# Kernel tuning notes

Hardware: AMD Instinct MI355X
Metric: run time of the kernel (lower is better)

Reference implementation:

```python
import jax, jax.numpy as jnp
import numpy as np

B, V, E = 64, 16384, 524288          # batch cells, genes (graph nodes), edges
CL1_F, CL1_K = 32, 6                  # cheby conv out-features, polynomial order
POOL = 8
FC1Fin = CL1_F * (V // POOL)          # 65536
FC1_F, FC2_F = 512, 512
NN_FC1, NN_FC2 = 1024, 512
OUT = 10


def _linear_params(k, fout, fin):
    k1, k2 = jax.random.split(k)
    s = 1.0 / np.sqrt(fin)
    w = jax.random.uniform(k1, (fout, fin), minval=-s, maxval=s, dtype=jnp.float32)
    b = jax.random.uniform(k2, (fout,), minval=-s, maxval=s, dtype=jnp.float32)
    return w, b


def setup_inputs() -> dict:
    key = jax.random.key(0)
    ks = jax.random.split(key, 12)
    cl1_w, cl1_b = _linear_params(ks[0], CL1_F, CL1_K)
    fc1_w, fc1_b = _linear_params(ks[1], FC1_F, FC1Fin)
    fc2_w, fc2_b = _linear_params(ks[2], FC2_F, FC1_F)
    fc3_w, fc3_b = _linear_params(ks[3], V, FC2_F)
    nn1_w, nn1_b = _linear_params(ks[4], NN_FC1, V)
    nn2_w, nn2_b = _linear_params(ks[5], NN_FC2, NN_FC1)
    sum2_w, sum2_b = _linear_params(ks[6], OUT, FC1_F + NN_FC2)
    x_in = jax.random.normal(ks[7], (B, V), dtype=jnp.float32)
    L_rows = jax.random.randint(ks[8], (E,), 0, V, dtype=jnp.int32)
    L_cols = jax.random.randint(ks[9], (E,), 0, V, dtype=jnp.int32)
    # values of the rescaled Laplacian 2L/lmax - I (preprocessing done on host)
    L_vals = jax.random.normal(ks[10], (E,), dtype=jnp.float32) * 0.01
    return dict(x_in=x_in, L_vals=L_vals,
                cl1_w=cl1_w, cl1_b=cl1_b, fc1_w=fc1_w, fc1_b=fc1_b,
                fc2_w=fc2_w, fc2_b=fc2_b, fc3_w=fc3_w, fc3_b=fc3_b,
                nn1_w=nn1_w, nn1_b=nn1_b, nn2_w=nn2_w, nn2_b=nn2_b,
                sum2_w=sum2_w, sum2_b=sum2_b,
                L_rows=L_rows, L_cols=L_cols)


def _spmm(vals, rows, cols, x):
    # sparse [V,V] @ dense [V,B] via gather + segment_sum
    return jax.ops.segment_sum(vals[:, None] * x[cols], rows, num_segments=V)


def reference(x_in, L_vals, cl1_w, cl1_b, fc1_w, fc1_b, fc2_w, fc2_b,
              fc3_w, fc3_b, nn1_w, nn1_b, nn2_w, nn2_b, sum2_w, sum2_b,
              L_rows, L_cols):
    # --- graph_conv_cheby (Fin = 1) ---
    x0 = x_in.T                      # [V, B]  (== view of [V, Fin*B])
    xs = [x0]
    x1 = _spmm(L_vals, L_rows, L_cols, x0)
    xs.append(x1)
    for _ in range(2, CL1_K):
        x2 = 2.0 * _spmm(L_vals, L_rows, L_cols, x1) - x0
        xs.append(x2)
        x0, x1 = x1, x2
    xc = jnp.stack(xs, 0)            # [K, V, B]
    xc = xc.transpose(2, 1, 0)       # [B, V, K]
    x = xc @ cl1_w.T + cl1_b         # [B, V, CL1_F]
    x = jax.nn.relu(x)
    # --- graph_max_pool(p=8) over node dim ---
    x = x.reshape(B, V // POOL, POOL, CL1_F).max(axis=2)   # [B, V/8, CL1_F]
    x = x.reshape(B, FC1Fin)
    # --- GAE hidden + decode branch ---
    x_hidden = jax.nn.relu(x @ fc1_w.T + fc1_b)            # [B, FC1_F]
    xd = jax.nn.relu(x_hidden @ fc2_w.T + fc2_b)           # FC2_F != 0 path
    # Dropout(d) with d=0 -> identity (deterministic reference)
    x_decode = xd @ fc3_w.T + fc3_b                        # [B, V]
    # --- plain NN branch on raw input ---
    xn = jax.nn.relu(x_in @ nn1_w.T + nn1_b)
    xn = jax.nn.relu(xn @ nn2_w.T + nn2_b)                 # [B, NN_FC2]
    # --- fuse + classify ---
    xcat = jnp.concatenate([x_hidden, xn], axis=1)
    logp = jax.nn.log_softmax(xcat @ sum2_w.T + sum2_b, axis=1)  # [B, OUT]
    return x_decode, x_hidden, logp
```

## Files before the change

kernel.cpp:

```cpp
#include <hip/hip_runtime.h>

#define B_    64
#define V_    16384
#define E_    524288
#define KCH   6
#define FCH   32
#define FIN1  65536
#define FC1F  512
#define FC2F  512
#define NN1F  1024
#define NN2F  512
#define OUTC  10
#define KT2   64

#define OFF_XS      0u
#define OFF_SCOL    12582912u
#define OFF_SVAL    13631488u
#define OFF_RSTART  14680064u
#define OFF_CNT     14746112u
#define OFF_CF      14811648u
#define OFF_SLICE   15073792u
#define OFF_XD      15073792u
#define OFF_XN1     15204864u
#define OFF_XN2     15467008u

typedef __attribute__((ext_vector_type(4))) float v4f;
typedef __attribute__((ext_vector_type(2))) float v2f;
typedef __attribute__((ext_vector_type(4))) unsigned short u16x4;

__device__ __forceinline__ float b2f(unsigned short h) {
    union { unsigned int u; float f; } v; v.u = ((unsigned int)h) << 16; return v.f;
}
__device__ __forceinline__ unsigned short f2b(float f) {
    union { float f; unsigned int u; } v; v.f = f;
    unsigned int u = v.u;
    u += 0x7fffu + ((u >> 16) & 1u);
    return (unsigned short)(u >> 16);
}

__global__ void prep_k(const float* __restrict__ xin, unsigned short* __restrict__ x0) {
    __shared__ unsigned short tl[64][65];
    int t = threadIdx.x;
    int v0 = blockIdx.x * 64;
    #pragma unroll
    for (int i = 0; i < 16; i++) {
        int idx = t + i * 256;
        int b = idx >> 6, v = idx & 63;
        tl[v][b] = f2b(xin[(size_t)b * V_ + v0 + v]);
    }
    __syncthreads();
    #pragma unroll
    for (int i = 0; i < 16; i++) {
        int idx = t + i * 256;
        int v = idx >> 6, b = idx & 63;
        x0[(size_t)(v0 + v) * B_ + b] = tl[v][b];
    }
}

__global__ void count_k(const int* __restrict__ rows, int* __restrict__ cnt) {
    int e = blockIdx.x * 256 + threadIdx.x;
    if (e < E_) atomicAdd(&cnt[rows[e] & (V_ - 1)], 1);
}

__global__ void scan_k(int* __restrict__ cnt_cursor, int* __restrict__ row_start) {
    __shared__ int sums[256];
    int t = threadIdx.x;
    int loc[64];
    int s = 0;
    #pragma unroll
    for (int i = 0; i < 64; i++) { loc[i] = cnt_cursor[t * 64 + i]; s += loc[i]; }
    sums[t] = s;
    __syncthreads();
    for (int off = 1; off < 256; off <<= 1) {
        int v = (t >= off) ? sums[t - off] : 0;
        __syncthreads();
        sums[t] += v;
        __syncthreads();
    }
    int base = (t == 0) ? 0 : sums[t - 1];
    #pragma unroll
    for (int i = 0; i < 64; i++) {
        row_start[t * 64 + i] = base;
        cnt_cursor[t * 64 + i] = base;
        base += loc[i];
    }
    if (t == 255) row_start[V_] = base;
}

__global__ void scatter_k(const int* __restrict__ rows, const int* __restrict__ cols,
                          const float* __restrict__ vals,
                          int* __restrict__ cursor, unsigned short* __restrict__ scol,
                          unsigned short* __restrict__ sval) {
    int e = blockIdx.x * 256 + threadIdx.x;
    if (e < E_) {
        int r = rows[e] & (V_ - 1);
        int p = atomicAdd(&cursor[r], 1);
        scol[p] = (unsigned short)(cols[e] & (V_ - 1));
        sval[p] = f2b(vals[e]);
    }
}

__global__ void spmm_k(const int* __restrict__ row_start, const unsigned short* __restrict__ scol,
                       const unsigned short* __restrict__ sval,
                       const unsigned short* __restrict__ x,
                       const unsigned short* __restrict__ xprev, unsigned short* __restrict__ y,
                       int mode) {
    int row  = blockIdx.x * 4 + (threadIdx.x >> 6);
    int lane = threadIdx.x & 63;
    int s = row_start[row], e = row_start[row + 1];
    float a0 = 0.f, a1 = 0.f, a2 = 0.f, a3 = 0.f;
    int i = s;
    for (; i + 4 <= e; i += 4) {
        int c0 = scol[i], c1 = scol[i + 1], c2 = scol[i + 2], c3 = scol[i + 3];
        float v0 = b2f(sval[i]), v1 = b2f(sval[i + 1]);
        float v2 = b2f(sval[i + 2]), v3 = b2f(sval[i + 3]);
        a0 += v0 * b2f(x[(size_t)c0 * B_ + lane]);
        a1 += v1 * b2f(x[(size_t)c1 * B_ + lane]);
        a2 += v2 * b2f(x[(size_t)c2 * B_ + lane]);
        a3 += v3 * b2f(x[(size_t)c3 * B_ + lane]);
    }
    for (; i < e; i++)
        a0 += b2f(sval[i]) * b2f(x[(size_t)scol[i] * B_ + lane]);
    float acc = (a0 + a1) + (a2 + a3);
    size_t o = (size_t)row * B_ + lane;
    float r = mode ? (2.f * acc - b2f(xprev[o])) : acc;
    y[o] = f2b(r);
}

__global__ void cheby_slice_k(const unsigned short* __restrict__ xs, const float* __restrict__ w,
                              const float* __restrict__ bias, unsigned short* __restrict__ slice,
                              int g) {
    __shared__ float tile[KCH * 512];
    __shared__ float wf[FCH * KCH];
    __shared__ float bf[FCH];
    int t = threadIdx.x;
    int vpl = blockIdx.x;
    int vp = g * 256 + vpl;
    for (int i = t; i < KCH * 512; i += 256) {
        int k = i >> 9, rem = i & 511;
        tile[i] = b2f(xs[(size_t)k * V_ * B_ + (size_t)vp * 512 + rem]);
    }
    if (t < FCH * KCH) wf[t] = w[t];
    if (t < FCH) bf[t] = bias[t];
    __syncthreads();
    int f = t & 31, b0 = t >> 5;
    float wr[KCH];
    #pragma unroll
    for (int k = 0; k < KCH; k++) wr[k] = wf[f * KCH + k];
    float bb = bf[f];
    #pragma unroll
    for (int bi = 0; bi < 8; bi++) {
        int b = b0 * 8 + bi;
        float m = -1e30f;
        #pragma unroll
        for (int j = 0; j < 8; j++) {
            float s = bb;
            #pragma unroll
            for (int k = 0; k < KCH; k++) s += tile[k * 512 + j * 64 + b] * wr[k];
            m = fmaxf(m, s);
        }
        slice[(size_t)b * 8192 + vpl * FCH + f] = f2b(fmaxf(m, 0.f));
    }
}

__global__ void gemm3_k(const void* __restrict__ Av, int a32, int lda, int ka0,
                        const float* __restrict__ W, int ldw, int kw0,
                        int klen, int N, const float* __restrict__ bias,
                        int relu, int direct, int accum,
                        float* __restrict__ Cp, float* __restrict__ Co) {
    __shared__ float As[KT2][68];
    __shared__ float Ws[KT2][36];
    const unsigned short* Au = (const unsigned short*)Av;
    const float* Af = (const float*)Av;
    int t = threadIdx.x;
    int nb = blockIdx.x * 32;
    int ka = ka0 + blockIdx.y * klen;
    int kw = kw0 + blockIdx.y * klen;
    int kq = t & 15;
    int r0 = t >> 4;
    int tm = (t & 31) << 1;
    int tn = (t >> 5) << 2;
    float acc[2][4] = {{0.f, 0.f, 0.f, 0.f}, {0.f, 0.f, 0.f, 0.f}};
    for (int kt = 0; kt < klen; kt += KT2) {
        __syncthreads();
        int kk = kq << 2;
        #pragma unroll
        for (int p = 0; p < 4; p++) {
            int row = r0 + p * 16;
            float a0, a1, a2, a3;
            if (a32) {
                v4f v = *(const v4f*)(Af + (size_t)row * lda + ka + kt + kk);
                a0 = v[0]; a1 = v[1]; a2 = v[2]; a3 = v[3];
            } else {
                u16x4 h = *(const u16x4*)(Au + (size_t)row * lda + ka + kt + kk);
                a0 = b2f(h[0]); a1 = b2f(h[1]); a2 = b2f(h[2]); a3 = b2f(h[3]);
            }
            As[kk + 0][row] = a0; As[kk + 1][row] = a1;
            As[kk + 2][row] = a2; As[kk + 3][row] = a3;
        }
        #pragma unroll
        for (int p = 0; p < 2; p++) {
            int row = r0 + p * 16;
            v4f w = *(const v4f*)(W + (size_t)(nb + row) * ldw + kw + kt + kk);
            Ws[kk + 0][row] = w[0]; Ws[kk + 1][row] = w[1];
            Ws[kk + 2][row] = w[2]; Ws[kk + 3][row] = w[3];
        }
        __syncthreads();
        #pragma unroll 8
        for (int k = 0; k < KT2; k++) {
            v2f a = *(const v2f*)&As[k][tm];
            v4f w = *(const v4f*)&Ws[k][tn];
            #pragma unroll
            for (int i = 0; i < 2; i++)
                #pragma unroll
                for (int j = 0; j < 4; j++)
                    acc[i][j] += a[i] * w[j];
        }
    }
    if (direct) {
        #pragma unroll
        for (int i = 0; i < 2; i++) {
            int m = tm + i;
            v4f v;
            #pragma unroll
            for (int j = 0; j < 4; j++) {
                float x = acc[i][j] + bias[nb + tn + j];
                v[j] = relu ? fmaxf(x, 0.f) : x;
            }
            *(v4f*)(Co + (size_t)m * N + nb + tn) = v;
        }
    } else {
        float* base = Cp + (size_t)blockIdx.y * 64 * N;
        #pragma unroll
        for (int i = 0; i < 2; i++) {
            int m = tm + i;
            float* p = base + (size_t)m * N + nb + tn;
            v4f v;
            if (accum) {
                v4f old = *(const v4f*)p;
                #pragma unroll
                for (int j = 0; j < 4; j++) v[j] = old[j] + acc[i][j];
            } else {
                #pragma unroll
                for (int j = 0; j < 4; j++) v[j] = acc[i][j];
            }
            *(v4f*)p = v;
        }
    }
}

__global__ void finish2_k(const float* __restrict__ Cp, int Y, int len,
                          const float* __restrict__ bias, int nmask, int relu,
                          float* __restrict__ o) {
    int i = blockIdx.x * 256 + threadIdx.x;
    float s = bias[i & nmask];
    for (int y = 0; y < Y; y++) s += Cp[(size_t)y * len + i];
    if (relu) s = fmaxf(s, 0.f);
    o[i] = s;
}

__global__ void sum2_k(const float* __restrict__ xh, const float* __restrict__ xn,
                       const float* __restrict__ w, const float* __restrict__ bias,
                       float* __restrict__ out) {
    int b = blockIdx.x;
    int lane = threadIdx.x;
    float xc[16];
    #pragma unroll
    for (int j = 0; j < 8; j++) xc[j] = xh[b * FC1F + j * 64 + lane];
    #pragma unroll
    for (int j = 0; j < 8; j++) xc[8 + j] = xn[b * NN2F + j * 64 + lane];
    float logits[OUTC];
    #pragma unroll
    for (int o = 0; o < OUTC; o++) {
        float s = 0.f;
        #pragma unroll
        for (int j = 0; j < 16; j++) s += xc[j] * w[o * 1024 + j * 64 + lane];
        #pragma unroll
        for (int off = 32; off; off >>= 1) s += __shfl_xor(s, off);
        logits[o] = s + bias[o];
    }
    float mx = logits[0];
    #pragma unroll
    for (int o = 1; o < OUTC; o++) mx = fmaxf(mx, logits[o]);
    float lse = 0.f;
    #pragma unroll
    for (int o = 0; o < OUTC; o++) lse += expf(logits[o] - mx);
    float lg = logf(lse) + mx;
    if (lane < OUTC) out[b * OUTC + lane] = logits[lane] - lg;
}

extern "C" void kernel_launch(void* const* d_in, const int* in_sizes, int n_in,
                              void* d_out, int out_size, void* d_ws, size_t ws_size,
                              hipStream_t stream) {
    const float* x_in   = (const float*)d_in[0];
    const float* L_vals = (const float*)d_in[1];
    const float* cl1_w  = (const float*)d_in[2];
    const float* cl1_b  = (const float*)d_in[3];
    const float* fc1_w  = (const float*)d_in[4];
    const float* fc1_b  = (const float*)d_in[5];
    const float* fc2_w  = (const float*)d_in[6];
    const float* fc2_b  = (const float*)d_in[7];
    const float* fc3_w  = (const float*)d_in[8];
    const float* fc3_b  = (const float*)d_in[9];
    const float* nn1_w  = (const float*)d_in[10];
    const float* nn1_b  = (const float*)d_in[11];
    const float* nn2_w  = (const float*)d_in[12];
    const float* nn2_b  = (const float*)d_in[13];
    const float* sum2_w = (const float*)d_in[14];
    const float* sum2_b = (const float*)d_in[15];
    const int* L_rows = (const int*)d_in[16];
    const int* L_cols = (const int*)d_in[17];
    float* out = (float*)d_out;
    char* ws = (char*)d_ws;

    unsigned short* xs     = (unsigned short*)(ws + OFF_XS);
    unsigned short* scol   = (unsigned short*)(ws + OFF_SCOL);
    unsigned short* sval   = (unsigned short*)(ws + OFF_SVAL);
    int*            rstart = (int*)(ws + OFF_RSTART);
    int*            cnt    = (int*)(ws + OFF_CNT);
    unsigned short* slice  = (unsigned short*)(ws + OFF_SLICE);
    float*          xd     = (float*)(ws + OFF_XD);
    float*          xn1    = (float*)(ws + OFF_XN1);
    float*          xn2    = (float*)(ws + OFF_XN2);
    float*          cp_a   = (float*)(ws + OFF_SCOL);
    float*          cp_b   = (float*)(ws + OFF_XS);

    float* out_decode = out;
    float* out_hidden = out + (size_t)B_ * V_;
    float* out_logp   = out_hidden + B_ * FC1F;

    prep_k<<<V_ / 64, 256, 0, stream>>>(x_in, xs);

    hipMemsetAsync(cnt, 0, V_ * sizeof(int), stream);
    count_k<<<E_ / 256, 256, 0, stream>>>(L_rows, cnt);
    scan_k<<<1, 256, 0, stream>>>(cnt, rstart);
    scatter_k<<<E_ / 256, 256, 0, stream>>>(L_rows, L_cols, L_vals, cnt, scol, sval);

    size_t VB = (size_t)V_ * B_;
    spmm_k<<<V_ / 4, 256, 0, stream>>>(rstart, scol, sval, xs, nullptr, xs + VB, 0);
    for (int k = 2; k < KCH; k++)
        spmm_k<<<V_ / 4, 256, 0, stream>>>(rstart, scol, sval,
                                           xs + (k - 1) * VB, xs + (k - 2) * VB, xs + k * VB, 1);

    for (int g = 0; g < 8; g++) {
        cheby_slice_k<<<256, 256, 0, stream>>>(xs, cl1_w, cl1_b, slice, g);
        gemm3_k<<<dim3(FC1F / 32, 16), 256, 0, stream>>>(slice, 0, 8192, 0,
                                                         fc1_w, FIN1, g * 8192,
                                                         512, FC1F, nullptr, 0, 0, g ? 1 : 0,
                                                         cp_a, nullptr);
    }
    finish2_k<<<B_ * FC1F / 256, 256, 0, stream>>>(cp_a, 16, B_ * FC1F, fc1_b, FC1F - 1, 1, out_hidden);

    gemm3_k<<<dim3(FC2F / 32, 8), 256, 0, stream>>>(out_hidden, 1, FC1F, 0,
                                                    fc2_w, FC1F, 0,
                                                    64, FC2F, nullptr, 0, 0, 0, cp_a, nullptr);
    finish2_k<<<B_ * FC2F / 256, 256, 0, stream>>>(cp_a, 8, B_ * FC2F, fc2_b, FC2F - 1, 1, xd);

    gemm3_k<<<dim3(V_ / 32, 1), 256, 0, stream>>>(xd, 1, FC2F, 0,
                                                  fc3_w, FC2F, 0,
                                                  FC2F, V_, fc3_b, 0, 1, 0, nullptr, out_decode);

    gemm3_k<<<dim3(NN1F / 32, 32), 256, 0, stream>>>(x_in, 1, V_, 0,
                                                     nn1_w, V_, 0,
                                                     512, NN1F, nullptr, 0, 0, 0, cp_b, nullptr);
    finish2_k<<<B_ * NN1F / 256, 256, 0, stream>>>(cp_b, 32, B_ * NN1F, nn1_b, NN1F - 1, 1, xn1);

    gemm3_k<<<dim3(NN2F / 32, 16), 256, 0, stream>>>(xn1, 1, NN1F, 0,
                                                     nn2_w, NN1F, 0,
                                                     64, NN2F, nullptr, 0, 0, 0, cp_b, nullptr);
    finish2_k<<<B_ * NN2F / 256, 256, 0, stream>>>(cp_b, 16, B_ * NN2F, nn2_b, NN2F - 1, 1, xn2);

    sum2_k<<<B_, 64, 0, stream>>>(out_hidden, xn2, sum2_w, sum2_b, out_logp);
}
```

Baseline: 870.6 us.

## Merge pipeline into three cooperative persistent kernels synchronized with grid barriers

Replaces about thirty separate launches (prep, CSR build, five SpMM steps, the eight cheby/fc1 rounds, the back-end GEMMs and reductions) with three cooperative kernels of 512 blocks that move between stages through grid.sync. The split-K for fc1 is re-partitioned so each block keeps its accumulator in registers across all eight slices and writes its partials only once, with the reduction fused in. The aim is to remove launch gaps and per-round partial-sum traffic. In exchange, the SpMM and GEMM stages are limited to 512 resident blocks and pay for many grid barriers. The old launch sequence is kept as a fallback if a cooperative launch fails.

```diff
diff --git a/kernel.cpp b/kernel.cpp
--- a/kernel.cpp
+++ b/kernel.cpp
@@ -1,4 +1,7 @@
 #include <hip/hip_runtime.h>
+#include <hip/hip_cooperative_groups.h>
+
+namespace cg = cooperative_groups;
 
 #define B_    64
 #define V_    16384
@@ -18,7 +21,6 @@
 #define OFF_SVAL    13631488u
 #define OFF_RSTART  14680064u
 #define OFF_CNT     14746112u
-#define OFF_CF      14811648u
 #define OFF_SLICE   15073792u
 #define OFF_XD      15073792u
 #define OFF_XN1     15204864u
@@ -38,6 +40,367 @@
     return (unsigned short)(u >> 16);
 }
 
+template <int A32>
+__device__ __forceinline__ void gemm_block(const void* __restrict__ Av, int lda, int ka,
+                                           const float* __restrict__ W, int ldw, int kw,
+                                           int klen, int nb, char* smem,
+                                           float acc[2][4], int t) {
+    float* As = (float*)smem;
+    float* Ws = (float*)(smem + KT2 * 68 * 4);
+    const unsigned short* Au = (const unsigned short*)Av;
+    const float* Af = (const float*)Av;
+    int kq = t & 15, r0 = t >> 4;
+    int tm = (t & 31) << 1, tn = (t >> 5) << 2;
+    for (int kt = 0; kt < klen; kt += KT2) {
+        __syncthreads();
+        int kk = kq << 2;
+        #pragma unroll
+        for (int p = 0; p < 4; p++) {
+            int row = r0 + p * 16;
+            float a0, a1, a2, a3;
+            if (A32) {
+                v4f v = *(const v4f*)(Af + (size_t)row * lda + ka + kt + kk);
+                a0 = v[0]; a1 = v[1]; a2 = v[2]; a3 = v[3];
+            } else {
+                u16x4 h = *(const u16x4*)(Au + (size_t)row * lda + ka + kt + kk);
+                a0 = b2f(h[0]); a1 = b2f(h[1]); a2 = b2f(h[2]); a3 = b2f(h[3]);
+            }
+            As[(kk + 0) * 68 + row] = a0; As[(kk + 1) * 68 + row] = a1;
+            As[(kk + 2) * 68 + row] = a2; As[(kk + 3) * 68 + row] = a3;
+        }
+        #pragma unroll
+        for (int p = 0; p < 2; p++) {
+            int row = r0 + p * 16;
+            v4f w = *(const v4f*)(W + (size_t)(nb + row) * ldw + kw + kt + kk);
+            Ws[(kk + 0) * 36 + row] = w[0]; Ws[(kk + 1) * 36 + row] = w[1];
+            Ws[(kk + 2) * 36 + row] = w[2]; Ws[(kk + 3) * 36 + row] = w[3];
+        }
+        __syncthreads();
+        #pragma unroll 8
+        for (int k = 0; k < KT2; k++) {
+            v2f a = *(const v2f*)&As[k * 68 + tm];
+            v4f w = *(const v4f*)&Ws[k * 36 + tn];
+            #pragma unroll
+            for (int i = 0; i < 2; i++)
+                #pragma unroll
+                for (int j = 0; j < 4; j++)
+                    acc[i][j] += a[i] * w[j];
+        }
+    }
+}
+
+
+__global__ void __launch_bounds__(256, 2) front_coop_k(
+        const float* __restrict__ xin, const int* __restrict__ rows,
+        const int* __restrict__ cols, const float* __restrict__ vals,
+        unsigned short* __restrict__ xs, unsigned short* __restrict__ scol,
+        unsigned short* __restrict__ sval, int* __restrict__ rstart,
+        int* __restrict__ cnt) {
+    cg::grid_group grid = cg::this_grid();
+    int t = threadIdx.x;
+    int bx = blockIdx.x;
+    __shared__ __align__(16) unsigned short tl[64][66];
+    __shared__ int sums[256];
+
+    if (bx < 256) {
+        int v0 = bx * 64;
+        #pragma unroll
+        for (int i = 0; i < 16; i++) {
+            int idx = t + i * 256;
+            int b = idx >> 6, v = idx & 63;
+            tl[v][b] = f2b(xin[(size_t)b * V_ + v0 + v]);
+        }
+        __syncthreads();
+        #pragma unroll
+        for (int i = 0; i < 16; i++) {
+            int idx = t + i * 256;
+            int v = idx >> 6, b = idx & 63;
+            xs[(size_t)(v0 + v) * B_ + b] = tl[v][b];
+        }
+    } else if (bx < 320) {
+        cnt[(bx - 256) * 256 + t] = 0;
+    }
+    grid.sync();
+
+    {
+        int idx = bx * 256 + t;
+        #pragma unroll
+        for (int h = 0; h < 4; h++)
+            atomicAdd(&cnt[rows[idx + h * 131072] & (V_ - 1)], 1);
+    }
+    grid.sync();
+
+    if (bx == 0) {
+        int s = 0;
+        for (int i = 0; i < 64; i++) s += cnt[t * 64 + i];
+        sums[t] = s;
+        __syncthreads();
+        for (int off = 1; off < 256; off <<= 1) {
+            int v = (t >= off) ? sums[t - off] : 0;
+            __syncthreads();
+            sums[t] += v;
+            __syncthreads();
+        }
+        int base = (t == 0) ? 0 : sums[t - 1];
+        for (int i = 0; i < 64; i++) {
+            int idx = t * 64 + i;
+            int c = cnt[idx];
+            rstart[idx] = base;
+            cnt[idx] = base;
+            base += c;
+        }
+        if (t == 255) rstart[V_] = base;
+    }
+    grid.sync();
+
+    {
+        int idx = bx * 256 + t;
+        #pragma unroll
+        for (int h = 0; h < 4; h++) {
+            int e = idx + h * 131072;
+            int r = rows[e] & (V_ - 1);
+            int p = atomicAdd(&cnt[r], 1);
+            scol[p] = (unsigned short)(cols[e] & (V_ - 1));
+            sval[p] = f2b(vals[e]);
+        }
+    }
+    grid.sync();
+
+    size_t VB = (size_t)V_ * B_;
+    int lane = t & 63;
+    int w = t >> 6;
+    for (int k = 1; k < KCH; k++) {
+        const unsigned short* x = xs + (size_t)(k - 1) * VB;
+        const unsigned short* xprev = xs + (size_t)(k >= 2 ? k - 2 : 0) * VB;
+        unsigned short* y = xs + (size_t)k * VB;
+        for (int rr = 0; rr < 8; rr++) {
+            int row = bx * 32 + w * 8 + rr;
+            int s = rstart[row], e = rstart[row + 1];
+            float a0 = 0.f, a1 = 0.f, a2 = 0.f, a3 = 0.f;
+            int i = s;
+            for (; i + 4 <= e; i += 4) {
+                int c0 = scol[i], c1 = scol[i + 1], c2 = scol[i + 2], c3 = scol[i + 3];
+                float v0 = b2f(sval[i]), v1 = b2f(sval[i + 1]);
+                float v2 = b2f(sval[i + 2]), v3 = b2f(sval[i + 3]);
+                a0 += v0 * b2f(x[(size_t)c0 * B_ + lane]);
+                a1 += v1 * b2f(x[(size_t)c1 * B_ + lane]);
+                a2 += v2 * b2f(x[(size_t)c2 * B_ + lane]);
+                a3 += v3 * b2f(x[(size_t)c3 * B_ + lane]);
+            }
+            for (; i < e; i++)
+                a0 += b2f(sval[i]) * b2f(x[(size_t)scol[i] * B_ + lane]);
+            float acc = (a0 + a1) + (a2 + a3);
+            size_t o = (size_t)row * B_ + lane;
+            float r = (k >= 2) ? (2.f * acc - b2f(xprev[o])) : acc;
+            y[o] = f2b(r);
+        }
+        if (k < KCH - 1) grid.sync();
+    }
+}
+
+__global__ void __launch_bounds__(256, 2) fc1_coop_k(
+        const unsigned short* __restrict__ xs, const float* __restrict__ cw,
+        const float* __restrict__ cb, const float* __restrict__ fw,
+        const float* __restrict__ fb, unsigned short* __restrict__ slice,
+        float* __restrict__ cp, float* __restrict__ outh) {
+    cg::grid_group grid = cg::this_grid();
+    int t = threadIdx.x;
+    int bx = blockIdx.x;
+    __shared__ __align__(16) char smem[26624];
+    size_t VB = (size_t)V_ * B_;
+
+    float acc[2][4] = {{0.f, 0.f, 0.f, 0.f}, {0.f, 0.f, 0.f, 0.f}};
+    int nb = (bx & 15) * 32;
+    int y  = bx >> 4;
+
+    for (int g = 0; g < 8; g++) {
+        {
+            float* tile = (float*)smem;
+            float* wf   = tile + KCH * 512;
+            float* bf   = wf + FCH * KCH;
+            int vpl = bx >> 1;
+            int bhalf = bx & 1;
+            int vp = g * 256 + vpl;
+            for (int i = t; i < KCH * 512; i += 256) {
+                int k = i >> 9, rem = i & 511;
+                tile[i] = b2f(xs[(size_t)k * VB + (size_t)vp * 512 + rem]);
+            }
+            if (t < FCH * KCH) wf[t] = cw[t];
+            if (t < FCH) bf[t] = cb[t];
+            __syncthreads();
+            int f = t & 31, b0 = t >> 5;
+            float wr[KCH];
+            #pragma unroll
+            for (int k = 0; k < KCH; k++) wr[k] = wf[f * KCH + k];
+            float bb = bf[f];
+            #pragma unroll
+            for (int bi2 = 0; bi2 < 4; bi2++) {
+                int bi = bhalf * 4 + bi2;
+                int b = b0 * 8 + bi;
+                float m = -1e30f;
+                #pragma unroll
+                for (int j = 0; j < 8; j++) {
+                    float s = bb;
+                    #pragma unroll
+                    for (int k = 0; k < KCH; k++) s += tile[k * 512 + j * 64 + b] * wr[k];
+                    m = fmaxf(m, s);
+                }
+                slice[(size_t)b * 8192 + vpl * FCH + f] = f2b(fmaxf(m, 0.f));
+            }
+            __syncthreads();
+        }
+        grid.sync();
+        gemm_block<0>(slice, 8192, y * 256, fw, FIN1, g * 8192 + y * 256, 256, nb, smem, acc, t);
+        grid.sync();
+    }
+    {
+        int tm = (t & 31) << 1, tn = (t >> 5) << 2;
+        float* base = cp + (size_t)y * (64 * FC1F);
+        #pragma unroll
+        for (int i = 0; i < 2; i++) {
+            v4f v;
+            #pragma unroll
+            for (int j = 0; j < 4; j++) v[j] = acc[i][j];
+            *(v4f*)(base + (size_t)(tm + i) * FC1F + nb + tn) = v;
+        }
+    }
+    grid.sync();
+    {
+        int idx = bx * 256 + t;
+        if (idx < 64 * FC1F) {
+            float s = fb[idx & (FC1F - 1)];
+            for (int yy = 0; yy < 32; yy++) s += cp[(size_t)yy * (64 * FC1F) + idx];
+            outh[idx] = fmaxf(s, 0.f);
+        }
+    }
+}
+
+__global__ void __launch_bounds__(256, 2) back_coop_k(
+        const float* __restrict__ outh, const float* __restrict__ fc2w,
+        const float* __restrict__ fc2b, float* __restrict__ xd,
+        const float* __restrict__ fc3w, const float* __restrict__ fc3b,
+        float* __restrict__ outd, const float* __restrict__ xin,
+        const float* __restrict__ nn1w, const float* __restrict__ nn1b,
+        float* __restrict__ xn1, const float* __restrict__ nn2w,
+        const float* __restrict__ nn2b, float* __restrict__ xn2,
+        const float* __restrict__ s2w, const float* __restrict__ s2b,
+        float* __restrict__ logp, float* __restrict__ cpb) {
+    cg::grid_group grid = cg::this_grid();
+    int t = threadIdx.x;
+    int bx = blockIdx.x;
+    __shared__ __align__(16) char smem[26624];
+    int tm = (t & 31) << 1, tn = (t >> 5) << 2;
+
+    if (bx < 128) {
+        int nb = (bx & 15) * 32, y = bx >> 4;
+        float acc[2][4] = {{0.f, 0.f, 0.f, 0.f}, {0.f, 0.f, 0.f, 0.f}};
+        gemm_block<1>(outh, FC1F, y * 64, fc2w, FC1F, y * 64, 64, nb, smem, acc, t);
+        float* base = cpb + (size_t)y * (64 * FC2F);
+        #pragma unroll
+        for (int i = 0; i < 2; i++) {
+            v4f v;
+            #pragma unroll
+            for (int j = 0; j < 4; j++) v[j] = acc[i][j];
+            *(v4f*)(base + (size_t)(tm + i) * FC2F + nb + tn) = v;
+        }
+    }
+    grid.sync();
+    {
+        int idx = bx * 256 + t;
+        if (idx < 64 * FC2F) {
+            float s = fc2b[idx & (FC2F - 1)];
+            for (int yy = 0; yy < 8; yy++) s += cpb[(size_t)yy * (64 * FC2F) + idx];
+            xd[idx] = fmaxf(s, 0.f);
+        }
+    }
+    grid.sync();
+    {
+        int nb = bx * 32;
+        float acc[2][4] = {{0.f, 0.f, 0.f, 0.f}, {0.f, 0.f, 0.f, 0.f}};
+        gemm_block<1>(xd, FC2F, 0, fc3w, FC2F, 0, FC2F, nb, smem, acc, t);
+        #pragma unroll
+        for (int i = 0; i < 2; i++) {
+            v4f v;
+            #pragma unroll
+            for (int j = 0; j < 4; j++) v[j] = acc[i][j] + fc3b[nb + tn + j];
+            *(v4f*)(outd + (size_t)(tm + i) * V_ + nb + tn) = v;
+        }
+    }
+    {
+        int nb = (bx & 31) * 32, y = bx >> 5;
+        float acc[2][4] = {{0.f, 0.f, 0.f, 0.f}, {0.f, 0.f, 0.f, 0.f}};
+        gemm_block<1>(xin, V_, y * 1024, nn1w, V_, y * 1024, 1024, nb, smem, acc, t);
+        float* base = cpb + (size_t)y * (64 * NN1F);
+        #pragma unroll
+        for (int i = 0; i < 2; i++) {
+            v4f v;
+            #pragma unroll
+            for (int j = 0; j < 4; j++) v[j] = acc[i][j];
+            *(v4f*)(base + (size_t)(tm + i) * NN1F + nb + tn) = v;
+        }
+    }
+    grid.sync();
+    {
+        int idx = bx * 256 + t;
+        if (idx < 64 * NN1F) {
+            float s = nn1b[idx & (NN1F - 1)];
+            for (int yy = 0; yy < 16; yy++) s += cpb[(size_t)yy * (64 * NN1F) + idx];
+            xn1[idx] = fmaxf(s, 0.f);
+        }
+    }
+    grid.sync();
+    if (bx < 256) {
+        int nb = (bx & 15) * 32, y = bx >> 4;
+        float acc[2][4] = {{0.f, 0.f, 0.f, 0.f}, {0.f, 0.f, 0.f, 0.f}};
+        gemm_block<1>(xn1, NN1F, y * 64, nn2w, NN1F, y * 64, 64, nb, smem, acc, t);
+        float* base = cpb + (size_t)y * (64 * NN2F);
+        #pragma unroll
+        for (int i = 0; i < 2; i++) {
+            v4f v;
+            #pragma unroll
+            for (int j = 0; j < 4; j++) v[j] = acc[i][j];
+            *(v4f*)(base + (size_t)(tm + i) * NN2F + nb + tn) = v;
+        }
+    }
+    grid.sync();
+    {
+        int idx = bx * 256 + t;
+        if (idx < 64 * NN2F) {
+            float s = nn2b[idx & (NN2F - 1)];
+            for (int yy = 0; yy < 16; yy++) s += cpb[(size_t)yy * (64 * NN2F) + idx];
+            xn2[idx] = fmaxf(s, 0.f);
+        }
+    }
+    grid.sync();
+    if (bx < 64 && t < 64) {
+        int b = bx, lane = t;
+        float xc[16];
+        #pragma unroll
+        for (int j = 0; j < 8; j++) xc[j] = outh[b * FC1F + j * 64 + lane];
+        #pragma unroll
+        for (int j = 0; j < 8; j++) xc[8 + j] = xn2[b * NN2F + j * 64 + lane];
+        float logits[OUTC];
+        #pragma unroll
+        for (int o = 0; o < OUTC; o++) {
+            float s = 0.f;
+            #pragma unroll
+            for (int j = 0; j < 16; j++) s += xc[j] * s2w[o * 1024 + j * 64 + lane];
+            #pragma unroll
+            for (int off = 32; off; off >>= 1) s += __shfl_xor(s, off);
+            logits[o] = s + s2b[o];
+        }
+        float mx = logits[0];
+        #pragma unroll
+        for (int o = 1; o < OUTC; o++) mx = fmaxf(mx, logits[o]);
+        float lse = 0.f;
+        #pragma unroll
+        for (int o = 0; o < OUTC; o++) lse += expf(logits[o] - mx);
+        float lg = logf(lse) + mx;
+        if (lane < OUTC) logp[b * OUTC + lane] = logits[lane] - lg;
+    }
+}
+
+
 __global__ void prep_k(const float* __restrict__ xin, unsigned short* __restrict__ x0) {
     __shared__ unsigned short tl[64][65];
     int t = threadIdx.x;
@@ -65,10 +428,8 @@
 __global__ void scan_k(int* __restrict__ cnt_cursor, int* __restrict__ row_start) {
     __shared__ int sums[256];
     int t = threadIdx.x;
-    int loc[64];
     int s = 0;
-    #pragma unroll
-    for (int i = 0; i < 64; i++) { loc[i] = cnt_cursor[t * 64 + i]; s += loc[i]; }
+    for (int i = 0; i < 64; i++) s += cnt_cursor[t * 64 + i];
     sums[t] = s;
     __syncthreads();
     for (int off = 1; off < 256; off <<= 1) {
@@ -78,11 +439,12 @@
         __syncthreads();
     }
     int base = (t == 0) ? 0 : sums[t - 1];
-    #pragma unroll
     for (int i = 0; i < 64; i++) {
-        row_start[t * 64 + i] = base;
-        cnt_cursor[t * 64 + i] = base;
-        base += loc[i];
+        int idx = t * 64 + i;
+        int c = cnt_cursor[idx];
+        row_start[idx] = base;
+        cnt_cursor[idx] = base;
+        base += c;
     }
     if (t == 255) row_start[V_] = base;
 }
@@ -168,55 +530,15 @@
                         int klen, int N, const float* __restrict__ bias,
                         int relu, int direct, int accum,
                         float* __restrict__ Cp, float* __restrict__ Co) {
-    __shared__ float As[KT2][68];
-    __shared__ float Ws[KT2][36];
-    const unsigned short* Au = (const unsigned short*)Av;
-    const float* Af = (const float*)Av;
+    __shared__ __align__(16) char smem[26624];
     int t = threadIdx.x;
     int nb = blockIdx.x * 32;
     int ka = ka0 + blockIdx.y * klen;
     int kw = kw0 + blockIdx.y * klen;
-    int kq = t & 15;
-    int r0 = t >> 4;
-    int tm = (t & 31) << 1;
-    int tn = (t >> 5) << 2;
+    int tm = (t & 31) << 1, tn = (t >> 5) << 2;
     float acc[2][4] = {{0.f, 0.f, 0.f, 0.f}, {0.f, 0.f, 0.f, 0.f}};
-    for (int kt = 0; kt < klen; kt += KT2) {
-        __syncthreads();
-        int kk = kq << 2;
-        #pragma unroll
-        for (int p = 0; p < 4; p++) {
-            int row = r0 + p * 16;
-            float a0, a1, a2, a3;
-            if (a32) {
-                v4f v = *(const v4f*)(Af + (size_t)row * lda + ka + kt + kk);
-                a0 = v[0]; a1 = v[1]; a2 = v[2]; a3 = v[3];
-            } else {
-                u16x4 h = *(const u16x4*)(Au + (size_t)row * lda + ka + kt + kk);
-                a0 = b2f(h[0]); a1 = b2f(h[1]); a2 = b2f(h[2]); a3 = b2f(h[3]);
-            }
-            As[kk + 0][row] = a0; As[kk + 1][row] = a1;
-            As[kk + 2][row] = a2; As[kk + 3][row] = a3;
-        }
-        #pragma unroll
-        for (int p = 0; p < 2; p++) {
-            int row = r0 + p * 16;
-            v4f w = *(const v4f*)(W + (size_t)(nb + row) * ldw + kw + kt + kk);
-            Ws[kk + 0][row] = w[0]; Ws[kk + 1][row] = w[1];
-            Ws[kk + 2][row] = w[2]; Ws[kk + 3][row] = w[3];
-        }
-        __syncthreads();
-        #pragma unroll 8
-        for (int k = 0; k < KT2; k++) {
-            v2f a = *(const v2f*)&As[k][tm];
-            v4f w = *(const v4f*)&Ws[k][tn];
-            #pragma unroll
-            for (int i = 0; i < 2; i++)
-                #pragma unroll
-                for (int j = 0; j < 4; j++)
-                    acc[i][j] += a[i] * w[j];
-        }
-    }
+    if (a32) gemm_block<1>(Av, lda, ka, W, ldw, kw, klen, nb, smem, acc, t);
+    else     gemm_block<0>(Av, lda, ka, W, ldw, kw, klen, nb, smem, acc, t);
     if (direct) {
         #pragma unroll
         for (int i = 0; i < 2; i++) {
@@ -323,52 +645,79 @@
     float*          xn1    = (float*)(ws + OFF_XN1);
     float*          xn2    = (float*)(ws + OFF_XN2);
     float*          cp_a   = (float*)(ws + OFF_SCOL);
-    float*          cp_b   = (float*)(ws + OFF_XS);
+    float*          cpb    = (float*)(ws + OFF_XS);
 
     float* out_decode = out;
     float* out_hidden = out + (size_t)B_ * V_;
     float* out_logp   = out_hidden + B_ * FC1F;
-
-    prep_k<<<V_ / 64, 256, 0, stream>>>(x_in, xs);
-
-    hipMemsetAsync(cnt, 0, V_ * sizeof(int), stream);
-    count_k<<<E_ / 256, 256, 0, stream>>>(L_rows, cnt);
-    scan_k<<<1, 256, 0, stream>>>(cnt, rstart);
-    scatter_k<<<E_ / 256, 256, 0, stream>>>(L_rows, L_cols, L_vals, cnt, scol, sval);
+    float* cp_fc1     = out_decode;
 
     size_t VB = (size_t)V_ * B_;
-    spmm_k<<<V_ / 4, 256, 0, stream>>>(rstart, scol, sval, xs, nullptr, xs + VB, 0);
-    for (int k = 2; k < KCH; k++)
-        spmm_k<<<V_ / 4, 256, 0, stream>>>(rstart, scol, sval,
-                                           xs + (k - 1) * VB, xs + (k - 2) * VB, xs + k * VB, 1);
-
-    for (int g = 0; g < 8; g++) {
-        cheby_slice_k<<<256, 256, 0, stream>>>(xs, cl1_w, cl1_b, slice, g);
-        gemm3_k<<<dim3(FC1F / 32, 16), 256, 0, stream>>>(slice, 0, 8192, 0,
-                                                         fc1_w, FIN1, g * 8192,
-                                                         512, FC1F, nullptr, 0, 0, g ? 1 : 0,
-                                                         cp_a, nullptr);
-    }
-    finish2_k<<<B_ * FC1F / 256, 256, 0, stream>>>(cp_a, 16, B_ * FC1F, fc1_b, FC1F - 1, 1, out_hidden);
-
-    gemm3_k<<<dim3(FC2F / 32, 8), 256, 0, stream>>>(out_hidden, 1, FC1F, 0,
-                                                    fc2_w, FC1F, 0,
-                                                    64, FC2F, nullptr, 0, 0, 0, cp_a, nullptr);
-    finish2_k<<<B_ * FC2F / 256, 256, 0, stream>>>(cp_a, 8, B_ * FC2F, fc2_b, FC2F - 1, 1, xd);
-
-    gemm3_k<<<dim3(V_ / 32, 1), 256, 0, stream>>>(xd, 1, FC2F, 0,
-                                                  fc3_w, FC2F, 0,
-                                                  FC2F, V_, fc3_b, 0, 1, 0, nullptr, out_decode);
-
-    gemm3_k<<<dim3(NN1F / 32, 32), 256, 0, stream>>>(x_in, 1, V_, 0,
-                                                     nn1_w, V_, 0,
-                                                     512, NN1F, nullptr, 0, 0, 0, cp_b, nullptr);
-    finish2_k<<<B_ * NN1F / 256, 256, 0, stream>>>(cp_b, 32, B_ * NN1F, nn1_b, NN1F - 1, 1, xn1);
-
-    gemm3_k<<<dim3(NN2F / 32, 16), 256, 0, stream>>>(xn1, 1, NN1F, 0,
-                                                     nn2_w, NN1F, 0,
-                                                     64, NN2F, nullptr, 0, 0, 0, cp_b, nullptr);
-    finish2_k<<<B_ * NN2F / 256, 256, 0, stream>>>(cp_b, 16, B_ * NN2F, nn2_b, NN2F - 1, 1, xn2);
-
-    sum2_k<<<B_, 64, 0, stream>>>(out_hidden, xn2, sum2_w, sum2_b, out_logp);
-}
+    bool front_done = false, fc1_done = false, back_done = false;
+
+    {
+        void* args[] = {(void*)&x_in, (void*)&L_rows, (void*)&L_cols, (void*)&L_vals,
+                        (void*)&xs, (void*)&scol, (void*)&sval, (void*)&rstart, (void*)&cnt};
+        if (hipLaunchCooperativeKernel((const void*)front_coop_k, dim3(512), dim3(256),
+                                       args, 0, stream) == hipSuccess)
+            front_done = true;
+    }
+    if (front_done) {
+        void* args[] = {(void*)&xs, (void*)&cl1_w, (void*)&cl1_b, (void*)&fc1_w, (void*)&fc1_b,
+                        (void*)&slice, (void*)&cp_fc1, (void*)&out_hidden};
+        if (hipLaunchCooperativeKernel((const void*)fc1_coop_k, dim3(512), dim3(256),
+                                       args, 0, stream) == hipSuccess)
+            fc1_done = true;
+    }
+    if (fc1_done) {
+        void* args[] = {(void*)&out_hidden, (void*)&fc2_w, (void*)&fc2_b, (void*)&xd,
+                        (void*)&fc3_w, (void*)&fc3_b, (void*)&out_decode, (void*)&x_in,
+                        (void*)&nn1_w, (void*)&nn1_b, (void*)&xn1,
+                        (void*)&nn2_w, (void*)&nn2_b, (void*)&xn2,
+                        (void*)&sum2_w, (void*)&sum2_b, (void*)&out_logp, (void*)&cpb};
+        if (hipLaunchCooperativeKernel((const void*)back_coop_k, dim3(512), dim3(256),
+                                       args, 0, stream) == hipSuccess)
+            back_done = true;
+    }
+
+    if (!front_done) {
+        prep_k<<<V_ / 64, 256, 0, stream>>>(x_in, xs);
+        hipMemsetAsync(cnt, 0, V_ * sizeof(int), stream);
+        count_k<<<E_ / 256, 256, 0, stream>>>(L_rows, cnt);
+        scan_k<<<1, 256, 0, stream>>>(cnt, rstart);
+        scatter_k<<<E_ / 256, 256, 0, stream>>>(L_rows, L_cols, L_vals, cnt, scol, sval);
+        spmm_k<<<V_ / 4, 256, 0, stream>>>(rstart, scol, sval, xs, nullptr, xs + VB, 0);
+        for (int k = 2; k < KCH; k++)
+            spmm_k<<<V_ / 4, 256, 0, stream>>>(rstart, scol, sval,
+                                               xs + (k - 1) * VB, xs + (k - 2) * VB, xs + k * VB, 1);
+    }
+    if (!fc1_done) {
+        for (int g = 0; g < 8; g++) {
+            cheby_slice_k<<<256, 256, 0, stream>>>(xs, cl1_w, cl1_b, slice, g);
+            gemm3_k<<<dim3(FC1F / 32, 16), 256, 0, stream>>>(slice, 0, 8192, 0,
+                                                             fc1_w, FIN1, g * 8192,
+                                                             512, FC1F, nullptr, 0, 0, g ? 1 : 0,
+                                                             cp_a, nullptr);
+        }
+        finish2_k<<<B_ * FC1F / 256, 256, 0, stream>>>(cp_a, 16, B_ * FC1F, fc1_b, FC1F - 1, 1,
+                                                       out_hidden);
+    }
+    if (!back_done) {
+        gemm3_k<<<dim3(FC2F / 32, 8), 256, 0, stream>>>(out_hidden, 1, FC1F, 0,
+                                                        fc2_w, FC1F, 0,
+                                                        64, FC2F, nullptr, 0, 0, 0, cp_a, nullptr);
+        finish2_k<<<B_ * FC2F / 256, 256, 0, stream>>>(cp_a, 8, B_ * FC2F, fc2_b, FC2F - 1, 1, xd);
+        gemm3_k<<<dim3(V_ / 32, 1), 256, 0, stream>>>(xd, 1, FC2F, 0,
+                                                      fc3_w, FC2F, 0,
+                                                      FC2F, V_, fc3_b, 0, 1, 0, nullptr, out_decode);
+        gemm3_k<<<dim3(NN1F / 32, 32), 256, 0, stream>>>(x_in, 1, V_, 0,
+                                                         nn1_w, V_, 0,
+                                                         512, NN1F, nullptr, 0, 0, 0, cpb, nullptr);
+        finish2_k<<<B_ * NN1F / 256, 256, 0, stream>>>(cpb, 32, B_ * NN1F, nn1_b, NN1F - 1, 1, xn1);
+        gemm3_k<<<dim3(NN2F / 32, 16), 256, 0, stream>>>(xn1, 1, NN1F, 0,
+                                                         nn2_w, NN1F, 0,
+                                                         64, NN2F, nullptr, 0, 0, 0, cpb, nullptr);
+        finish2_k<<<B_ * NN2F / 256, 256, 0, stream>>>(cpb, 16, B_ * NN2F, nn2_b, NN2F - 1, 1, xn2);
+        sum2_k<<<B_, 64, 0, stream>>>(out_hidden, xn2, sum2_w, sum2_b, out_logp);
+    }
+}
```

Result: slower. 2.592 ms (+197.7%).
